# Kernel optimization log

Measured on AMD Instinct MI355X. Metric: run time of the kernel, lower is better.

Reference implementation:

```python
import jax, jax.numpy as jnp
import numpy as np

NUM_GRAPHS = 512


def _sage_conv(x, src, tgt, num_nodes, w_n, b_n, w_r):
    # PyG SAGEConv with mean aggregation:
    #   out = mean_{j in N(i)} x_j @ w_n + b_n + x_i @ w_r
    msgs = x[src]                                   # [E, d] gather
    agg = jax.ops.segment_sum(msgs, tgt, num_segments=num_nodes)   # [N, d]
    deg = jax.ops.segment_sum(jnp.ones((src.shape[0],), x.dtype), tgt,
                              num_segments=num_nodes)              # [N]
    agg = agg / jnp.maximum(deg, 1.0)[:, None]
    return agg @ w_n + b_n + x @ w_r


def setup_inputs() -> dict:
    key = jax.random.key(0)
    ks = jax.random.split(key, 10)
    N, E, D_IN, D_H, D_OUT = 50000, 800000, 128, 128, 10
    s = 0.05
    x = jax.random.normal(ks[0], (N, D_IN), dtype=jnp.float32)
    edge_index = jax.random.randint(ks[1], (2, E), 0, N, dtype=jnp.int64)
    batch = jnp.sort(jax.random.randint(ks[2], (N,), 0, NUM_GRAPHS, dtype=jnp.int64))
    return {
        "x": x,
        "edge_index": edge_index,
        "batch": batch,
        "w1_n": jax.random.normal(ks[3], (D_IN, D_H), dtype=jnp.float32) * s,
        "b1": jnp.zeros((D_H,), jnp.float32),
        "w1_r": jax.random.normal(ks[4], (D_IN, D_H), dtype=jnp.float32) * s,
        "w2_n": jax.random.normal(ks[5], (D_H, D_H), dtype=jnp.float32) * s,
        "b2": jnp.zeros((D_H,), jnp.float32),
        "w2_r": jax.random.normal(ks[6], (D_H, D_H), dtype=jnp.float32) * s,
        "fc_w": jax.random.normal(ks[7], (D_H, D_OUT), dtype=jnp.float32) * s,
        "fc_b": jnp.zeros((D_OUT,), jnp.float32),
    }


def reference(x, edge_index, batch, w1_n, b1, w1_r, w2_n, b2, w2_r, fc_w, fc_b):
    N = x.shape[0]
    src, tgt = edge_index[0], edge_index[1]
    h = _sage_conv(x, src, tgt, N, w1_n, b1, w1_r)
    h = jax.nn.relu(h)  # dropout is identity in eval mode
    h = _sage_conv(h, src, tgt, N, w2_n, b2, w2_r)
    # global_mean_pool over graph ids
    pooled = jax.ops.segment_sum(h, batch, num_segments=NUM_GRAPHS)
    cnt = jax.ops.segment_sum(jnp.ones((N,), h.dtype), batch, num_segments=NUM_GRAPHS)
    pooled = pooled / jnp.maximum(cnt, 1.0)[:, None]
    return pooled @ fc_w + fc_b
```

## Files before the change

kernel.cpp:

```cpp
#include <hip/hip_runtime.h>

#define D 128
#define G_NUM 512

typedef unsigned short u16;
typedef __attribute__((ext_vector_type(8))) short bf16x8;
typedef __attribute__((ext_vector_type(4))) float f32x4;

__device__ __forceinline__ float bf2f(u16 u) {
    return __uint_as_float(((unsigned int)u) << 16);
}
__device__ __forceinline__ u16 f2bf_rne(float f) {
    unsigned int u = __float_as_uint(f);
    unsigned int r = (u + 0x7FFFu + ((u >> 16) & 1u)) >> 16;
    return (u16)r;
}
__device__ __forceinline__ void split_bf16(float v, u16& h, u16& l) {
    h = f2bf_rne(v);
    l = f2bf_rne(v - bf2f(h));
}

__global__ void deg_kernel(const int* __restrict__ tgt, int* __restrict__ deg, int E) {
    int e = blockIdx.x * blockDim.x + threadIdx.x;
    if (e < E) atomicAdd(&deg[tgt[e]], 1);
}

__global__ void scan1_kernel(const int* __restrict__ deg, int* __restrict__ row_excl,
                             int* __restrict__ partial, int N) {
    __shared__ int s[256];
    int t = threadIdx.x, i = blockIdx.x * 256 + t;
    int v = (i < N) ? deg[i] : 0;
    s[t] = v;
    __syncthreads();
    for (int off = 1; off < 256; off <<= 1) {
        int add = (t >= off) ? s[t - off] : 0;
        __syncthreads();
        s[t] += add;
        __syncthreads();
    }
    if (i < N) row_excl[i] = s[t] - v;
    if (t == 255) partial[blockIdx.x] = s[255];
}

__global__ void scan2_kernel(int* __restrict__ partial, int NB) {
    __shared__ int s[256];
    int t = threadIdx.x;
    int v = (t < NB) ? partial[t] : 0;
    s[t] = v;
    __syncthreads();
    for (int off = 1; off < 256; off <<= 1) {
        int add = (t >= off) ? s[t - off] : 0;
        __syncthreads();
        s[t] += add;
        __syncthreads();
    }
    if (t < NB) partial[t] = s[t] - v;
}

__global__ void scan3_kernel(int* __restrict__ row_start, const int* __restrict__ partial,
                             int* __restrict__ deg, float* __restrict__ rdeg, int N, int E) {
    int i = blockIdx.x * blockDim.x + threadIdx.x;
    if (i < N) {
        row_start[i] += partial[blockIdx.x];
        float d = (float)deg[i];
        rdeg[i] = 1.0f / fmaxf(d, 1.0f);
        deg[i] = 0;
    }
    if (i == 0) row_start[N] = E;
}

__global__ void fill_kernel(const int* __restrict__ src, const int* __restrict__ tgt,
                            const int* __restrict__ row_start, int* __restrict__ cursor,
                            int* __restrict__ col_idx, int E) {
    int e = blockIdx.x * blockDim.x + threadIdx.x;
    if (e >= E) return;
    int t = tgt[e];
    int pos = row_start[t] + atomicAdd(&cursor[t], 1);
    col_idx[pos] = src[e];
}

__global__ void boundary_kernel(const int* __restrict__ batch, int* __restrict__ gstart, int N) {
    int i = blockIdx.x * blockDim.x + threadIdx.x;
    if (i >= N) return;
    int b = batch[i];
    int bp = (i == 0) ? -1 : batch[i - 1];
    for (int g = bp + 1; g <= b; g++) gstart[g] = i;
    if (i == N - 1)
        for (int g = b + 1; g <= G_NUM; g++) gstart[g] = N;
}

__global__ void convert_x_kernel(const float* __restrict__ x, u16* __restrict__ xh,
                                 u16* __restrict__ xl, int n4) {
    int i = blockIdx.x * blockDim.x + threadIdx.x;
    if (i >= n4) return;
    float4 v = ((const float4*)x)[i];
    ushort4 h, l;
    split_bf16(v.x, h.x, l.x);
    split_bf16(v.y, h.y, l.y);
    split_bf16(v.z, h.z, l.z);
    split_bf16(v.w, h.w, l.w);
    ((ushort4*)xh)[i] = h;
    ((ushort4*)xl)[i] = l;
}

__global__ void convert_w_kernel(const float* __restrict__ w0, const float* __restrict__ w1,
                                 const float* __restrict__ w2, const float* __restrict__ w3,
                                 u16* __restrict__ wp) {
    int t = blockIdx.x * blockDim.x + threadIdx.x;
    if (t >= 8192) return;
    int g = t & 3, c = (t >> 2) & 127, kt = (t >> 9) & 3, mat = t >> 11;
    const float* W = (mat == 0) ? w0 : (mat == 1) ? w1 : (mat == 2) ? w2 : w3;
    u16* dh = wp + mat * 32768 + ((size_t)(kt * 128 + c) * 4 + g) * 8;
    u16* dl = dh + 16384;
#pragma unroll
    for (int j = 0; j < 8; j++) {
        float v = W[(size_t)(kt * 32 + g * 8 + j) * D + c];
        u16 h, l;
        split_bf16(v, h, l);
        dh[j] = h;
        dl[j] = l;
    }
}

template <int BF16IN>
__global__ __launch_bounds__(256) void gather_kernel(
    const int* __restrict__ row_start, const int* __restrict__ col_idx,
    const float* __restrict__ rdeg, const float* __restrict__ feat32,
    const u16* __restrict__ fhi, const u16* __restrict__ flo,
    u16* __restrict__ agg_hi, u16* __restrict__ agg_lo, int N) {
    int node = blockIdx.x * 8 + (threadIdx.x >> 5);
    if (node >= N) return;
    int q = threadIdx.x & 31;
    int beg = row_start[node], end = row_start[node + 1];
    float ax = 0.f, ay = 0.f, az = 0.f, aw = 0.f;
    int i = beg;
    for (; i + 4 <= end; i += 4) {
        int s0 = col_idx[i], s1 = col_idx[i + 1], s2 = col_idx[i + 2], s3 = col_idx[i + 3];
        if (BF16IN) {
            ushort4 h0 = *(const ushort4*)(fhi + (size_t)s0 * D + q * 4);
            ushort4 l0 = *(const ushort4*)(flo + (size_t)s0 * D + q * 4);
            ushort4 h1 = *(const ushort4*)(fhi + (size_t)s1 * D + q * 4);
            ushort4 l1 = *(const ushort4*)(flo + (size_t)s1 * D + q * 4);
            ushort4 h2 = *(const ushort4*)(fhi + (size_t)s2 * D + q * 4);
            ushort4 l2 = *(const ushort4*)(flo + (size_t)s2 * D + q * 4);
            ushort4 h3 = *(const ushort4*)(fhi + (size_t)s3 * D + q * 4);
            ushort4 l3 = *(const ushort4*)(flo + (size_t)s3 * D + q * 4);
            ax += bf2f(h0.x) + bf2f(l0.x) + bf2f(h1.x) + bf2f(l1.x) +
                  bf2f(h2.x) + bf2f(l2.x) + bf2f(h3.x) + bf2f(l3.x);
            ay += bf2f(h0.y) + bf2f(l0.y) + bf2f(h1.y) + bf2f(l1.y) +
                  bf2f(h2.y) + bf2f(l2.y) + bf2f(h3.y) + bf2f(l3.y);
            az += bf2f(h0.z) + bf2f(l0.z) + bf2f(h1.z) + bf2f(l1.z) +
                  bf2f(h2.z) + bf2f(l2.z) + bf2f(h3.z) + bf2f(l3.z);
            aw += bf2f(h0.w) + bf2f(l0.w) + bf2f(h1.w) + bf2f(l1.w) +
                  bf2f(h2.w) + bf2f(l2.w) + bf2f(h3.w) + bf2f(l3.w);
        } else {
            float4 v0 = ((const float4*)feat32)[(size_t)s0 * 32 + q];
            float4 v1 = ((const float4*)feat32)[(size_t)s1 * 32 + q];
            float4 v2 = ((const float4*)feat32)[(size_t)s2 * 32 + q];
            float4 v3 = ((const float4*)feat32)[(size_t)s3 * 32 + q];
            ax += v0.x + v1.x + v2.x + v3.x;
            ay += v0.y + v1.y + v2.y + v3.y;
            az += v0.z + v1.z + v2.z + v3.z;
            aw += v0.w + v1.w + v2.w + v3.w;
        }
    }
    for (; i < end; i++) {
        int s = col_idx[i];
        if (BF16IN) {
            ushort4 h = *(const ushort4*)(fhi + (size_t)s * D + q * 4);
            ushort4 l = *(const ushort4*)(flo + (size_t)s * D + q * 4);
            ax += bf2f(h.x) + bf2f(l.x);
            ay += bf2f(h.y) + bf2f(l.y);
            az += bf2f(h.z) + bf2f(l.z);
            aw += bf2f(h.w) + bf2f(l.w);
        } else {
            float4 v = ((const float4*)feat32)[(size_t)s * 32 + q];
            ax += v.x;
            ay += v.y;
            az += v.z;
            aw += v.w;
        }
    }
    float rd = rdeg[node];
    ax *= rd; ay *= rd; az *= rd; aw *= rd;
    ushort4 hv, lv;
    split_bf16(ax, hv.x, lv.x);
    split_bf16(ay, hv.y, lv.y);
    split_bf16(az, hv.z, lv.z);
    split_bf16(aw, hv.w, lv.w);
    *(ushort4*)(agg_hi + (size_t)node * D + q * 4) = hv;
    *(ushort4*)(agg_lo + (size_t)node * D + q * 4) = lv;
}

template <int MODE>
__global__ __launch_bounds__(256) void mfma_gemm_kernel(
    const u16* __restrict__ Ah, const u16* __restrict__ Al,
    const u16* __restrict__ Xh, const u16* __restrict__ Xl,
    const u16* __restrict__ Wnh, const u16* __restrict__ Wnl,
    const u16* __restrict__ Wrh, const u16* __restrict__ Wrl,
    const float* __restrict__ bias, float* __restrict__ out_f32,
    u16* __restrict__ out_hi, u16* __restrict__ out_lo, int N) {
    int wave = threadIdx.x >> 6;
    int lane = threadIdx.x & 63;
    int row0 = blockIdx.x * 64 + wave * 16;
    int r = lane & 15, g = lane >> 4;

    int arow = min(row0 + r, N - 1);
    size_t abase = (size_t)arow * D + g * 8;

    f32x4 acc[8];
#pragma unroll
    for (int ct = 0; ct < 8; ct++) acc[ct] = (f32x4){0.f, 0.f, 0.f, 0.f};

#pragma unroll
    for (int kt = 0; kt < 4; kt++) {
        bf16x8 ah = *(const bf16x8*)(Ah + abase + kt * 32);
        bf16x8 al = *(const bf16x8*)(Al + abase + kt * 32);
        bf16x8 xh = *(const bf16x8*)(Xh + abase + kt * 32);
        bf16x8 xl = *(const bf16x8*)(Xl + abase + kt * 32);
        size_t wb = ((size_t)(kt * 128 + r) * 4 + g) * 8;
#pragma unroll
        for (int ct = 0; ct < 8; ct++) {
            size_t wo = wb + (size_t)ct * 512;
            bf16x8 bnh = *(const bf16x8*)(Wnh + wo);
            bf16x8 bnl = *(const bf16x8*)(Wnl + wo);
            bf16x8 brh = *(const bf16x8*)(Wrh + wo);
            bf16x8 brl = *(const bf16x8*)(Wrl + wo);
            acc[ct] = __builtin_amdgcn_mfma_f32_16x16x32_bf16(ah, bnh, acc[ct], 0, 0, 0);
            acc[ct] = __builtin_amdgcn_mfma_f32_16x16x32_bf16(al, bnh, acc[ct], 0, 0, 0);
            acc[ct] = __builtin_amdgcn_mfma_f32_16x16x32_bf16(ah, bnl, acc[ct], 0, 0, 0);
            acc[ct] = __builtin_amdgcn_mfma_f32_16x16x32_bf16(xh, brh, acc[ct], 0, 0, 0);
            acc[ct] = __builtin_amdgcn_mfma_f32_16x16x32_bf16(xl, brh, acc[ct], 0, 0, 0);
            acc[ct] = __builtin_amdgcn_mfma_f32_16x16x32_bf16(xh, brl, acc[ct], 0, 0, 0);
        }
    }

#pragma unroll
    for (int ct = 0; ct < 8; ct++) {
        int col = ct * 16 + r;
        float bv = bias[col];
#pragma unroll
        for (int reg = 0; reg < 4; reg++) {
            int row = row0 + g * 4 + reg;
            if (row >= N) continue;
            float v = acc[ct][reg] + bv;
            if (MODE == 0) {
                v = fmaxf(v, 0.f);
                u16 h, l;
                split_bf16(v, h, l);
                out_hi[(size_t)row * D + col] = h;
                out_lo[(size_t)row * D + col] = l;
            } else {
                out_f32[(size_t)row * D + col] = v;
            }
        }
    }
}

__global__ __launch_bounds__(128) void pool_fc_kernel(
    const float* __restrict__ h2, const int* __restrict__ gstart,
    const float* __restrict__ fcw, const float* __restrict__ fcb, float* __restrict__ out) {
    __shared__ float p[D];
    int g = blockIdx.x, t = threadIdx.x;
    int s = gstart[g], e = gstart[g + 1];
    float acc = 0.f;
    for (int r = s; r < e; r++) acc += h2[(size_t)r * D + t];
    float rc = 1.0f / fmaxf((float)(e - s), 1.0f);
    p[t] = acc * rc;
    __syncthreads();
    if (t < 10) {
        float o = fcb[t];
#pragma unroll
        for (int k = 0; k < D; k++) o += p[k] * fcw[k * 10 + t];
        out[g * 10 + t] = o;
    }
}

extern "C" void kernel_launch(void* const* d_in, const int* in_sizes, int n_in,
                              void* d_out, int out_size, void* d_ws, size_t ws_size,
                              hipStream_t stream) {
    const float* x   = (const float*)d_in[0];
    const int*   ei  = (const int*)d_in[1];
    const int* batch = (const int*)d_in[2];
    const float* w1n = (const float*)d_in[3];
    const float* b1  = (const float*)d_in[4];
    const float* w1r = (const float*)d_in[5];
    const float* w2n = (const float*)d_in[6];
    const float* b2  = (const float*)d_in[7];
    const float* w2r = (const float*)d_in[8];
    const float* fcw = (const float*)d_in[9];
    const float* fcb = (const float*)d_in[10];
    float* out = (float*)d_out;

    int N = in_sizes[0] / D;
    int E = in_sizes[1] / 2;
    const int* src = ei;
    const int* tgt = ei + E;
    int NB = (N + 255) / 256;

    auto au = [](size_t v) { return (v + 255) & ~(size_t)255; };
    char* p = (char*)d_ws;
    int*   deg       = (int*)p;    p += au((size_t)N * 4);
    int*   row_start = (int*)p;    p += au((size_t)(N + 1) * 4);
    int*   partial   = (int*)p;    p += au(256 * 4);
    int*   col_idx   = (int*)p;    p += au((size_t)E * 4);
    float* rdeg      = (float*)p;  p += au((size_t)N * 4);
    int*   gstart    = (int*)p;    p += au((size_t)(G_NUM + 1) * 4);
    u16*   wp        = (u16*)p;    p += au((size_t)8 * 16384 * 2);
    u16*   xh        = (u16*)p;    p += au((size_t)N * D * 2);
    u16*   xl        = (u16*)p;    p += au((size_t)N * D * 2);
    u16*   aggh      = (u16*)p;    p += au((size_t)N * D * 2);
    u16*   aggl      = (u16*)p;    p += au((size_t)N * D * 2);
    u16*   h1h       = (u16*)p;    p += au((size_t)N * D * 2);
    u16*   h1l       = (u16*)p;    p += au((size_t)N * D * 2);
    float* h2        = (float*)xh;

    hipMemsetAsync(deg, 0, (size_t)N * 4, stream);

    deg_kernel<<<(E + 255) / 256, 256, 0, stream>>>(tgt, deg, E);
    scan1_kernel<<<NB, 256, 0, stream>>>(deg, row_start, partial, N);
    scan2_kernel<<<1, 256, 0, stream>>>(partial, NB);
    scan3_kernel<<<NB, 256, 0, stream>>>(row_start, partial, deg, rdeg, N, E);
    fill_kernel<<<(E + 255) / 256, 256, 0, stream>>>(src, tgt, row_start, deg, col_idx, E);

    convert_x_kernel<<<(N * 32 + 255) / 256, 256, 0, stream>>>(x, xh, xl, N * 32);
    convert_w_kernel<<<32, 256, 0, stream>>>(w1n, w1r, w2n, w2r, wp);
    boundary_kernel<<<NB, 256, 0, stream>>>(batch, gstart, N);

    int gb = (N + 7) / 8;
    int mb = (N + 63) / 64;

    gather_kernel<0><<<gb, 256, 0, stream>>>(row_start, col_idx, rdeg, x, nullptr, nullptr,
                                             aggh, aggl, N);
    mfma_gemm_kernel<0><<<mb, 256, 0, stream>>>(aggh, aggl, xh, xl,
                                                wp + 0 * 32768, wp + 0 * 32768 + 16384,
                                                wp + 1 * 32768, wp + 1 * 32768 + 16384,
                                                b1, nullptr, h1h, h1l, N);

    gather_kernel<1><<<gb, 256, 0, stream>>>(row_start, col_idx, rdeg, nullptr, h1h, h1l,
                                             aggh, aggl, N);
    mfma_gemm_kernel<1><<<mb, 256, 0, stream>>>(aggh, aggl, h1h, h1l,
                                                wp + 2 * 32768, wp + 2 * 32768 + 16384,
                                                wp + 3 * 32768, wp + 3 * 32768 + 16384,
                                                b2, h2, nullptr, nullptr, N);

    pool_fc_kernel<<<G_NUM, 128, 0, stream>>>(h2, gstart, fcw, fcb, out);
}
```

Before: 442.0 us.

## Fuse prep kernels, pack hidden features, and make GEMM persistent with register-resident weights

Merges the x conversion, degree counting, weight conversion and graph-boundary kernels into one launch to cut launch overhead. Stores layer-1 output as packed hi/lo u32 pairs so the second gather issues one 16-byte load per neighbor instead of two 8-byte loads. Restructures the GEMM into a persistent grid where each wave keeps its two column tiles of weights in registers and loops over 16-row tiles, removing repeated weight loads. This raises register pressure and adds repacking work inside the second GEMM.

```diff
diff --git a/kernel.cpp b/kernel.cpp
--- a/kernel.cpp
+++ b/kernel.cpp
@@ -4,25 +4,75 @@
 #define G_NUM 512
 
 typedef unsigned short u16;
+typedef unsigned int u32;
 typedef __attribute__((ext_vector_type(8))) short bf16x8;
 typedef __attribute__((ext_vector_type(4))) float f32x4;
 
 __device__ __forceinline__ float bf2f(u16 u) {
-    return __uint_as_float(((unsigned int)u) << 16);
+    return __uint_as_float(((u32)u) << 16);
 }
 __device__ __forceinline__ u16 f2bf_rne(float f) {
-    unsigned int u = __float_as_uint(f);
-    unsigned int r = (u + 0x7FFFu + ((u >> 16) & 1u)) >> 16;
+    u32 u = __float_as_uint(f);
+    u32 r = (u + 0x7FFFu + ((u >> 16) & 1u)) >> 16;
     return (u16)r;
 }
 __device__ __forceinline__ void split_bf16(float v, u16& h, u16& l) {
     h = f2bf_rne(v);
     l = f2bf_rne(v - bf2f(h));
 }
-
-__global__ void deg_kernel(const int* __restrict__ tgt, int* __restrict__ deg, int E) {
-    int e = blockIdx.x * blockDim.x + threadIdx.x;
-    if (e < E) atomicAdd(&deg[tgt[e]], 1);
+__device__ __forceinline__ float pk_hi(u32 u) { return __uint_as_float(u & 0xFFFF0000u); }
+__device__ __forceinline__ float pk_lo(u32 u) { return __uint_as_float(u << 16); }
+__device__ __forceinline__ bf16x8 mk8(u32 a, u32 b, u32 c, u32 d) {
+    union { u32 u[4]; bf16x8 v; } t;
+    t.u[0] = a; t.u[1] = b; t.u[2] = c; t.u[3] = d;
+    return t.v;
+}
+
+__global__ void prep_kernel(const float* __restrict__ x, u16* __restrict__ xh, u16* __restrict__ xl,
+                            const float* __restrict__ w0, const float* __restrict__ w1,
+                            const float* __restrict__ w2, const float* __restrict__ w3,
+                            u16* __restrict__ wp,
+                            const int* __restrict__ batch, int* __restrict__ gstart,
+                            const int* __restrict__ tgt, int* __restrict__ deg,
+                            int n4, int E, int N, int NBX, int NBE) {
+    int b = blockIdx.x, t = threadIdx.x;
+    if (b < NBX) {
+        int i = b * 256 + t;
+        if (i >= n4) return;
+        float4 v = ((const float4*)x)[i];
+        ushort4 h, l;
+        split_bf16(v.x, h.x, l.x);
+        split_bf16(v.y, h.y, l.y);
+        split_bf16(v.z, h.z, l.z);
+        split_bf16(v.w, h.w, l.w);
+        ((ushort4*)xh)[i] = h;
+        ((ushort4*)xl)[i] = l;
+    } else if (b < NBX + NBE) {
+        int e = (b - NBX) * 256 + t;
+        if (e < E) atomicAdd(&deg[tgt[e]], 1);
+    } else if (b < NBX + NBE + 32) {
+        int id = (b - NBX - NBE) * 256 + t;
+        int g = id & 3, c = (id >> 2) & 127, kt = (id >> 9) & 3, mat = id >> 11;
+        const float* W = (mat == 0) ? w0 : (mat == 1) ? w1 : (mat == 2) ? w2 : w3;
+        u16* dh = wp + mat * 32768 + ((size_t)(kt * 128 + c) * 4 + g) * 8;
+        u16* dl = dh + 16384;
+#pragma unroll
+        for (int j = 0; j < 8; j++) {
+            float v = W[(size_t)(kt * 32 + g * 8 + j) * D + c];
+            u16 h, l;
+            split_bf16(v, h, l);
+            dh[j] = h;
+            dl[j] = l;
+        }
+    } else {
+        int i = (b - NBX - NBE - 32) * 256 + t;
+        if (i >= N) return;
+        int bb = batch[i];
+        int bp = (i == 0) ? -1 : batch[i - 1];
+        for (int g = bp + 1; g <= bb; g++) gstart[g] = i;
+        if (i == N - 1)
+            for (int g = bb + 1; g <= G_NUM; g++) gstart[g] = N;
+    }
 }
 
 __global__ void scan1_kernel(const int* __restrict__ deg, int* __restrict__ row_excl,
@@ -79,54 +129,10 @@
     col_idx[pos] = src[e];
 }
 
-__global__ void boundary_kernel(const int* __restrict__ batch, int* __restrict__ gstart, int N) {
-    int i = blockIdx.x * blockDim.x + threadIdx.x;
-    if (i >= N) return;
-    int b = batch[i];
-    int bp = (i == 0) ? -1 : batch[i - 1];
-    for (int g = bp + 1; g <= b; g++) gstart[g] = i;
-    if (i == N - 1)
-        for (int g = b + 1; g <= G_NUM; g++) gstart[g] = N;
-}
-
-__global__ void convert_x_kernel(const float* __restrict__ x, u16* __restrict__ xh,
-                                 u16* __restrict__ xl, int n4) {
-    int i = blockIdx.x * blockDim.x + threadIdx.x;
-    if (i >= n4) return;
-    float4 v = ((const float4*)x)[i];
-    ushort4 h, l;
-    split_bf16(v.x, h.x, l.x);
-    split_bf16(v.y, h.y, l.y);
-    split_bf16(v.z, h.z, l.z);
-    split_bf16(v.w, h.w, l.w);
-    ((ushort4*)xh)[i] = h;
-    ((ushort4*)xl)[i] = l;
-}
-
-__global__ void convert_w_kernel(const float* __restrict__ w0, const float* __restrict__ w1,
-                                 const float* __restrict__ w2, const float* __restrict__ w3,
-                                 u16* __restrict__ wp) {
-    int t = blockIdx.x * blockDim.x + threadIdx.x;
-    if (t >= 8192) return;
-    int g = t & 3, c = (t >> 2) & 127, kt = (t >> 9) & 3, mat = t >> 11;
-    const float* W = (mat == 0) ? w0 : (mat == 1) ? w1 : (mat == 2) ? w2 : w3;
-    u16* dh = wp + mat * 32768 + ((size_t)(kt * 128 + c) * 4 + g) * 8;
-    u16* dl = dh + 16384;
-#pragma unroll
-    for (int j = 0; j < 8; j++) {
-        float v = W[(size_t)(kt * 32 + g * 8 + j) * D + c];
-        u16 h, l;
-        split_bf16(v, h, l);
-        dh[j] = h;
-        dl[j] = l;
-    }
-}
-
-template <int BF16IN>
+template <int PK>
 __global__ __launch_bounds__(256) void gather_kernel(
     const int* __restrict__ row_start, const int* __restrict__ col_idx,
-    const float* __restrict__ rdeg, const float* __restrict__ feat32,
-    const u16* __restrict__ fhi, const u16* __restrict__ flo,
+    const float* __restrict__ rdeg, const void* __restrict__ feat,
     u16* __restrict__ agg_hi, u16* __restrict__ agg_lo, int N) {
     int node = blockIdx.x * 8 + (threadIdx.x >> 5);
     if (node >= N) return;
@@ -136,28 +142,24 @@
     int i = beg;
     for (; i + 4 <= end; i += 4) {
         int s0 = col_idx[i], s1 = col_idx[i + 1], s2 = col_idx[i + 2], s3 = col_idx[i + 3];
-        if (BF16IN) {
-            ushort4 h0 = *(const ushort4*)(fhi + (size_t)s0 * D + q * 4);
-            ushort4 l0 = *(const ushort4*)(flo + (size_t)s0 * D + q * 4);
-            ushort4 h1 = *(const ushort4*)(fhi + (size_t)s1 * D + q * 4);
-            ushort4 l1 = *(const ushort4*)(flo + (size_t)s1 * D + q * 4);
-            ushort4 h2 = *(const ushort4*)(fhi + (size_t)s2 * D + q * 4);
-            ushort4 l2 = *(const ushort4*)(flo + (size_t)s2 * D + q * 4);
-            ushort4 h3 = *(const ushort4*)(fhi + (size_t)s3 * D + q * 4);
-            ushort4 l3 = *(const ushort4*)(flo + (size_t)s3 * D + q * 4);
-            ax += bf2f(h0.x) + bf2f(l0.x) + bf2f(h1.x) + bf2f(l1.x) +
-                  bf2f(h2.x) + bf2f(l2.x) + bf2f(h3.x) + bf2f(l3.x);
-            ay += bf2f(h0.y) + bf2f(l0.y) + bf2f(h1.y) + bf2f(l1.y) +
-                  bf2f(h2.y) + bf2f(l2.y) + bf2f(h3.y) + bf2f(l3.y);
-            az += bf2f(h0.z) + bf2f(l0.z) + bf2f(h1.z) + bf2f(l1.z) +
-                  bf2f(h2.z) + bf2f(l2.z) + bf2f(h3.z) + bf2f(l3.z);
-            aw += bf2f(h0.w) + bf2f(l0.w) + bf2f(h1.w) + bf2f(l1.w) +
-                  bf2f(h2.w) + bf2f(l2.w) + bf2f(h3.w) + bf2f(l3.w);
+        if (PK) {
+            uint4 v0 = ((const uint4*)feat)[(size_t)s0 * 32 + q];
+            uint4 v1 = ((const uint4*)feat)[(size_t)s1 * 32 + q];
+            uint4 v2 = ((const uint4*)feat)[(size_t)s2 * 32 + q];
+            uint4 v3 = ((const uint4*)feat)[(size_t)s3 * 32 + q];
+            ax += (pk_hi(v0.x) + pk_lo(v0.x)) + (pk_hi(v1.x) + pk_lo(v1.x)) +
+                  (pk_hi(v2.x) + pk_lo(v2.x)) + (pk_hi(v3.x) + pk_lo(v3.x));
+            ay += (pk_hi(v0.y) + pk_lo(v0.y)) + (pk_hi(v1.y) + pk_lo(v1.y)) +
+                  (pk_hi(v2.y) + pk_lo(v2.y)) + (pk_hi(v3.y) + pk_lo(v3.y));
+            az += (pk_hi(v0.z) + pk_lo(v0.z)) + (pk_hi(v1.z) + pk_lo(v1.z)) +
+                  (pk_hi(v2.z) + pk_lo(v2.z)) + (pk_hi(v3.z) + pk_lo(v3.z));
+            aw += (pk_hi(v0.w) + pk_lo(v0.w)) + (pk_hi(v1.w) + pk_lo(v1.w)) +
+                  (pk_hi(v2.w) + pk_lo(v2.w)) + (pk_hi(v3.w) + pk_lo(v3.w));
         } else {
-            float4 v0 = ((const float4*)feat32)[(size_t)s0 * 32 + q];
-            float4 v1 = ((const float4*)feat32)[(size_t)s1 * 32 + q];
-            float4 v2 = ((const float4*)feat32)[(size_t)s2 * 32 + q];
-            float4 v3 = ((const float4*)feat32)[(size_t)s3 * 32 + q];
+            float4 v0 = ((const float4*)feat)[(size_t)s0 * 32 + q];
+            float4 v1 = ((const float4*)feat)[(size_t)s1 * 32 + q];
+            float4 v2 = ((const float4*)feat)[(size_t)s2 * 32 + q];
+            float4 v3 = ((const float4*)feat)[(size_t)s3 * 32 + q];
             ax += v0.x + v1.x + v2.x + v3.x;
             ay += v0.y + v1.y + v2.y + v3.y;
             az += v0.z + v1.z + v2.z + v3.z;
@@ -166,15 +168,14 @@
     }
     for (; i < end; i++) {
         int s = col_idx[i];
-        if (BF16IN) {
-            ushort4 h = *(const ushort4*)(fhi + (size_t)s * D + q * 4);
-            ushort4 l = *(const ushort4*)(flo + (size_t)s * D + q * 4);
-            ax += bf2f(h.x) + bf2f(l.x);
-            ay += bf2f(h.y) + bf2f(l.y);
-            az += bf2f(h.z) + bf2f(l.z);
-            aw += bf2f(h.w) + bf2f(l.w);
+        if (PK) {
+            uint4 v = ((const uint4*)feat)[(size_t)s * 32 + q];
+            ax += pk_hi(v.x) + pk_lo(v.x);
+            ay += pk_hi(v.y) + pk_lo(v.y);
+            az += pk_hi(v.z) + pk_lo(v.z);
+            aw += pk_hi(v.w) + pk_lo(v.w);
         } else {
-            float4 v = ((const float4*)feat32)[(size_t)s * 32 + q];
+            float4 v = ((const float4*)feat)[(size_t)s * 32 + q];
             ax += v.x;
             ay += v.y;
             az += v.z;
@@ -192,66 +193,90 @@
     *(ushort4*)(agg_lo + (size_t)node * D + q * 4) = lv;
 }
 
-template <int MODE>
-__global__ __launch_bounds__(256) void mfma_gemm_kernel(
+template <int XP, int OUTM>
+__global__ __launch_bounds__(256, 2) void mfma_gemm_kernel(
     const u16* __restrict__ Ah, const u16* __restrict__ Al,
-    const u16* __restrict__ Xh, const u16* __restrict__ Xl,
+    const u16* __restrict__ Xh, const u16* __restrict__ Xl, const u32* __restrict__ Xp,
     const u16* __restrict__ Wnh, const u16* __restrict__ Wnl,
     const u16* __restrict__ Wrh, const u16* __restrict__ Wrl,
-    const float* __restrict__ bias, float* __restrict__ out_f32,
-    u16* __restrict__ out_hi, u16* __restrict__ out_lo, int N) {
+    const float* __restrict__ bias,
+    u32* __restrict__ out_pk, float* __restrict__ out_f32, int N, int NT) {
     int wave = threadIdx.x >> 6;
     int lane = threadIdx.x & 63;
-    int row0 = blockIdx.x * 64 + wave * 16;
     int r = lane & 15, g = lane >> 4;
-
-    int arow = min(row0 + r, N - 1);
-    size_t abase = (size_t)arow * D + g * 8;
-
-    f32x4 acc[8];
-#pragma unroll
-    for (int ct = 0; ct < 8; ct++) acc[ct] = (f32x4){0.f, 0.f, 0.f, 0.f};
-
-#pragma unroll
-    for (int kt = 0; kt < 4; kt++) {
-        bf16x8 ah = *(const bf16x8*)(Ah + abase + kt * 32);
-        bf16x8 al = *(const bf16x8*)(Al + abase + kt * 32);
-        bf16x8 xh = *(const bf16x8*)(Xh + abase + kt * 32);
-        bf16x8 xl = *(const bf16x8*)(Xl + abase + kt * 32);
-        size_t wb = ((size_t)(kt * 128 + r) * 4 + g) * 8;
-#pragma unroll
-        for (int ct = 0; ct < 8; ct++) {
-            size_t wo = wb + (size_t)ct * 512;
-            bf16x8 bnh = *(const bf16x8*)(Wnh + wo);
-            bf16x8 bnl = *(const bf16x8*)(Wnl + wo);
-            bf16x8 brh = *(const bf16x8*)(Wrh + wo);
-            bf16x8 brl = *(const bf16x8*)(Wrl + wo);
-            acc[ct] = __builtin_amdgcn_mfma_f32_16x16x32_bf16(ah, bnh, acc[ct], 0, 0, 0);
-            acc[ct] = __builtin_amdgcn_mfma_f32_16x16x32_bf16(al, bnh, acc[ct], 0, 0, 0);
-            acc[ct] = __builtin_amdgcn_mfma_f32_16x16x32_bf16(ah, bnl, acc[ct], 0, 0, 0);
-            acc[ct] = __builtin_amdgcn_mfma_f32_16x16x32_bf16(xh, brh, acc[ct], 0, 0, 0);
-            acc[ct] = __builtin_amdgcn_mfma_f32_16x16x32_bf16(xl, brh, acc[ct], 0, 0, 0);
-            acc[ct] = __builtin_amdgcn_mfma_f32_16x16x32_bf16(xh, brl, acc[ct], 0, 0, 0);
-        }
-    }
-
-#pragma unroll
-    for (int ct = 0; ct < 8; ct++) {
-        int col = ct * 16 + r;
-        float bv = bias[col];
+    int ctBase = wave * 2;
+
+    bf16x8 Bn[2][4][2], Br[2][4][2];
+#pragma unroll
+    for (int c2 = 0; c2 < 2; c2++)
+#pragma unroll
+        for (int kt = 0; kt < 4; kt++) {
+            size_t wo = ((size_t)(kt * 128 + r) * 4 + g) * 8 + (size_t)(ctBase + c2) * 512;
+            Bn[c2][kt][0] = *(const bf16x8*)(Wnh + wo);
+            Bn[c2][kt][1] = *(const bf16x8*)(Wnl + wo);
+            Br[c2][kt][0] = *(const bf16x8*)(Wrh + wo);
+            Br[c2][kt][1] = *(const bf16x8*)(Wrl + wo);
+        }
+    int col0 = ctBase * 16 + r, col1 = col0 + 16;
+    float bv0 = bias[col0], bv1 = bias[col1];
+
+    for (int rt = blockIdx.x; rt < NT; rt += gridDim.x) {
+        int row0 = rt * 16;
+        int arow = min(row0 + r, N - 1);
+        size_t abase = (size_t)arow * D + g * 8;
+        f32x4 acc0 = (f32x4){0.f, 0.f, 0.f, 0.f};
+        f32x4 acc1 = (f32x4){0.f, 0.f, 0.f, 0.f};
+#pragma unroll
+        for (int kt = 0; kt < 4; kt++) {
+            bf16x8 ah = *(const bf16x8*)(Ah + abase + kt * 32);
+            bf16x8 al = *(const bf16x8*)(Al + abase + kt * 32);
+            bf16x8 xh, xl;
+            if (XP == 0) {
+                xh = *(const bf16x8*)(Xh + abase + kt * 32);
+                xl = *(const bf16x8*)(Xl + abase + kt * 32);
+            } else {
+                const u32* xp = Xp + abase + kt * 32;
+                uint4 wa = *(const uint4*)(xp);
+                uint4 wb = *(const uint4*)(xp + 4);
+                xh = mk8((wa.y & 0xFFFF0000u) | (wa.x >> 16),
+                         (wa.w & 0xFFFF0000u) | (wa.z >> 16),
+                         (wb.y & 0xFFFF0000u) | (wb.x >> 16),
+                         (wb.w & 0xFFFF0000u) | (wb.z >> 16));
+                xl = mk8((wa.y << 16) | (wa.x & 0xFFFFu),
+                         (wa.w << 16) | (wa.z & 0xFFFFu),
+                         (wb.y << 16) | (wb.x & 0xFFFFu),
+                         (wb.w << 16) | (wb.z & 0xFFFFu));
+            }
+            acc0 = __builtin_amdgcn_mfma_f32_16x16x32_bf16(ah, Bn[0][kt][0], acc0, 0, 0, 0);
+            acc1 = __builtin_amdgcn_mfma_f32_16x16x32_bf16(ah, Bn[1][kt][0], acc1, 0, 0, 0);
+            acc0 = __builtin_amdgcn_mfma_f32_16x16x32_bf16(al, Bn[0][kt][0], acc0, 0, 0, 0);
+            acc1 = __builtin_amdgcn_mfma_f32_16x16x32_bf16(al, Bn[1][kt][0], acc1, 0, 0, 0);
+            acc0 = __builtin_amdgcn_mfma_f32_16x16x32_bf16(ah, Bn[0][kt][1], acc0, 0, 0, 0);
+            acc1 = __builtin_amdgcn_mfma_f32_16x16x32_bf16(ah, Bn[1][kt][1], acc1, 0, 0, 0);
+            acc0 = __builtin_amdgcn_mfma_f32_16x16x32_bf16(xh, Br[0][kt][0], acc0, 0, 0, 0);
+            acc1 = __builtin_amdgcn_mfma_f32_16x16x32_bf16(xh, Br[1][kt][0], acc1, 0, 0, 0);
+            acc0 = __builtin_amdgcn_mfma_f32_16x16x32_bf16(xl, Br[0][kt][0], acc0, 0, 0, 0);
+            acc1 = __builtin_amdgcn_mfma_f32_16x16x32_bf16(xl, Br[1][kt][0], acc1, 0, 0, 0);
+            acc0 = __builtin_amdgcn_mfma_f32_16x16x32_bf16(xh, Br[0][kt][1], acc0, 0, 0, 0);
+            acc1 = __builtin_amdgcn_mfma_f32_16x16x32_bf16(xh, Br[1][kt][1], acc1, 0, 0, 0);
+        }
 #pragma unroll
         for (int reg = 0; reg < 4; reg++) {
             int row = row0 + g * 4 + reg;
             if (row >= N) continue;
-            float v = acc[ct][reg] + bv;
-            if (MODE == 0) {
-                v = fmaxf(v, 0.f);
+            float v0 = acc0[reg] + bv0;
+            float v1 = acc1[reg] + bv1;
+            if (OUTM == 0) {
+                v0 = fmaxf(v0, 0.f);
+                v1 = fmaxf(v1, 0.f);
                 u16 h, l;
-                split_bf16(v, h, l);
-                out_hi[(size_t)row * D + col] = h;
-                out_lo[(size_t)row * D + col] = l;
+                split_bf16(v0, h, l);
+                out_pk[(size_t)row * D + col0] = ((u32)h << 16) | l;
+                split_bf16(v1, h, l);
+                out_pk[(size_t)row * D + col1] = ((u32)h << 16) | l;
             } else {
-                out_f32[(size_t)row * D + col] = v;
+                out_f32[(size_t)row * D + col0] = v0;
+                out_f32[(size_t)row * D + col1] = v1;
             }
         }
     }
@@ -311,38 +336,39 @@
     u16*   xl        = (u16*)p;    p += au((size_t)N * D * 2);
     u16*   aggh      = (u16*)p;    p += au((size_t)N * D * 2);
     u16*   aggl      = (u16*)p;    p += au((size_t)N * D * 2);
-    u16*   h1h       = (u16*)p;    p += au((size_t)N * D * 2);
-    u16*   h1l       = (u16*)p;    p += au((size_t)N * D * 2);
+    u32*   h1p       = (u32*)p;    p += au((size_t)N * D * 4);
     float* h2        = (float*)xh;
 
     hipMemsetAsync(deg, 0, (size_t)N * 4, stream);
 
-    deg_kernel<<<(E + 255) / 256, 256, 0, stream>>>(tgt, deg, E);
+    int n4 = N * 32;
+    int NBX = (n4 + 255) / 256;
+    int NBE = (E + 255) / 256;
+    prep_kernel<<<NBX + NBE + 32 + NB, 256, 0, stream>>>(
+        x, xh, xl, w1n, w1r, w2n, w2r, wp, batch, gstart, tgt, deg, n4, E, N, NBX, NBE);
+
     scan1_kernel<<<NB, 256, 0, stream>>>(deg, row_start, partial, N);
     scan2_kernel<<<1, 256, 0, stream>>>(partial, NB);
     scan3_kernel<<<NB, 256, 0, stream>>>(row_start, partial, deg, rdeg, N, E);
-    fill_kernel<<<(E + 255) / 256, 256, 0, stream>>>(src, tgt, row_start, deg, col_idx, E);
-
-    convert_x_kernel<<<(N * 32 + 255) / 256, 256, 0, stream>>>(x, xh, xl, N * 32);
-    convert_w_kernel<<<32, 256, 0, stream>>>(w1n, w1r, w2n, w2r, wp);
-    boundary_kernel<<<NB, 256, 0, stream>>>(batch, gstart, N);
+    fill_kernel<<<NBE, 256, 0, stream>>>(src, tgt, row_start, deg, col_idx, E);
 
     int gb = (N + 7) / 8;
-    int mb = (N + 63) / 64;
-
-    gather_kernel<0><<<gb, 256, 0, stream>>>(row_start, col_idx, rdeg, x, nullptr, nullptr,
-                                             aggh, aggl, N);
-    mfma_gemm_kernel<0><<<mb, 256, 0, stream>>>(aggh, aggl, xh, xl,
-                                                wp + 0 * 32768, wp + 0 * 32768 + 16384,
-                                                wp + 1 * 32768, wp + 1 * 32768 + 16384,
-                                                b1, nullptr, h1h, h1l, N);
-
-    gather_kernel<1><<<gb, 256, 0, stream>>>(row_start, col_idx, rdeg, nullptr, h1h, h1l,
-                                             aggh, aggl, N);
-    mfma_gemm_kernel<1><<<mb, 256, 0, stream>>>(aggh, aggl, h1h, h1l,
-                                                wp + 2 * 32768, wp + 2 * 32768 + 16384,
-                                                wp + 3 * 32768, wp + 3 * 32768 + 16384,
-                                                b2, h2, nullptr, nullptr, N);
+    int NT = (N + 15) / 16;
+    int gemm_grid = NT < 500 ? NT : 500;
+
+    gather_kernel<0><<<gb, 256, 0, stream>>>(row_start, col_idx, rdeg, x, aggh, aggl, N);
+    mfma_gemm_kernel<0, 0><<<gemm_grid, 256, 0, stream>>>(
+        aggh, aggl, xh, xl, nullptr,
+        wp + 0 * 32768, wp + 0 * 32768 + 16384,
+        wp + 1 * 32768, wp + 1 * 32768 + 16384,
+        b1, h1p, nullptr, N, NT);
+
+    gather_kernel<1><<<gb, 256, 0, stream>>>(row_start, col_idx, rdeg, h1p, aggh, aggl, N);
+    mfma_gemm_kernel<1, 1><<<gemm_grid, 256, 0, stream>>>(
+        aggh, aggl, nullptr, nullptr, h1p,
+        wp + 2 * 32768, wp + 2 * 32768 + 16384,
+        wp + 3 * 32768, wp + 3 * 32768 + 16384,
+        b2, nullptr, h2, N, NT);
 
     pool_fc_kernel<<<G_NUM, 128, 0, stream>>>(h2, gstart, fcw, fcb, out);
 }
```

After: 390.2 us. -11.7%, faster.
